# Performance work log

Hardware: AMD Instinct MI355X
Metric: run time of the kernel (lower is better)

Reference implementation:

```python
import jax, jax.numpy as jnp
import numpy as np

B, C, H, W = 2, 64, 128, 128
O = 64
DG = 8          # deformable groups
K = 3
KK = K * K
PAD = 1
MRM = 10.0      # max_residue_magnitude


def setup_inputs() -> dict:
    key = jax.random.key(0)
    ks = jax.random.split(key, 6)
    x0 = jax.random.normal(ks[0], (B, C, H, W), jnp.float32)
    x1 = jax.random.normal(ks[1], (B, C, H, W), jnp.float32)
    pre_offset = jax.random.normal(ks[2], (B, 2 * DG * KK, H, W), jnp.float32)
    pre_sim = jax.random.uniform(ks[3], (B, DG * KK, H, W), jnp.float32)
    stdv = 1.0 / float(np.sqrt(C * KK))
    weight = jax.random.uniform(ks[4], (O, C, K, K), jnp.float32, -stdv, stdv)
    bias = jnp.zeros((O,), jnp.float32)
    # conv_offset_mask params (zero-init in original; small random here so the path is exercised)
    w_om = jax.random.normal(ks[5], (3 * DG * KK, C, K, K), jnp.float32) * 0.01
    b_om = jnp.zeros((3 * DG * KK,), jnp.float32)
    return dict(x0=x0, x1=x1, pre_offset=pre_offset, pre_sim=pre_sim,
                weight=weight, bias=bias, w_om=w_om, b_om=b_om)


def _gather(xg, idx):
    # xg: [BG, cg, HW], idx: [BG, N] int32 -> [BG, cg, N]
    return jax.vmap(lambda a, i: a[:, i])(xg, idx)


def _modulated_deform_conv(x, offset, mask, weight, bias):
    b = x.shape[0]
    cg = C // DG
    # channel layout: ((g*KK + i)*2 + axis), axis 0 = y, 1 = x
    off = offset.reshape(b, DG, KK, 2, H, W)
    m = mask.reshape(b, DG, KK, H, W)
    ky = (jnp.arange(KK) // K).astype(jnp.float32)
    kx = (jnp.arange(KK) % K).astype(jnp.float32)
    base_h = jnp.arange(H, dtype=jnp.float32) - PAD   # stride 1
    base_w = jnp.arange(W, dtype=jnp.float32) - PAD
    py = off[:, :, :, 0] + base_h[None, None, None, :, None] + ky[None, None, :, None, None]
    px = off[:, :, :, 1] + base_w[None, None, None, None, :] + kx[None, None, :, None, None]
    y0 = jnp.floor(py); x0f = jnp.floor(px)
    ly = py - y0; lx = px - x0f
    hy = 1.0 - ly; hx = 1.0 - lx
    y0i = y0.astype(jnp.int32); x0i = x0f.astype(jnp.int32)
    xg = x.reshape(b * DG, cg, H * W)

    def corner(yi, xi, wgt):
        inb = (yi >= 0) & (yi < H) & (xi >= 0) & (xi < W)
        idx = jnp.clip(yi, 0, H - 1) * W + jnp.clip(xi, 0, W - 1)
        g = _gather(xg, idx.reshape(b * DG, KK * H * W))
        g = g.reshape(b, DG, cg, KK, H, W)
        return g * (wgt * inb.astype(x.dtype))[:, :, None]

    val = (corner(y0i, x0i, hy * hx) + corner(y0i, x0i + 1, hy * lx)
           + corner(y0i + 1, x0i, ly * hx) + corner(y0i + 1, x0i + 1, ly * lx))
    val = val * m[:, :, None]                       # modulation mask
    wr = weight.reshape(O, DG, cg, KK)
    out = jnp.einsum('bgckhw,ogck->bohw', val, wr)
    return out + bias[None, :, None, None]


def reference(x0, x1, pre_offset, pre_sim, weight, bias, w_om, b_om):
    # conv_offset_mask on the extra feature x1
    om = jax.lax.conv_general_dilated(x1, w_om, (1, 1), [(PAD, PAD), (PAD, PAD)],
                                      dimension_numbers=('NCHW', 'OIHW', 'NCHW'))
    om = om + b_om[None, :, None, None]
    o1, o2, msk = jnp.split(om, 3, axis=1)
    offset = MRM * jnp.tanh(jnp.concatenate([o1, o2], axis=1)) + pre_offset
    msk = jax.nn.sigmoid(msk * pre_sim)
    return _modulated_deform_conv(x0, offset, msk, weight, bias)
```

## Files before the change

kernel.cpp:

```cpp
#include <hip/hip_runtime.h>
#include <hip/hip_bf16.h>
#include <math.h>

constexpr int B  = 2;
constexpr int C  = 64;
constexpr int H  = 128;
constexpr int W  = 128;
constexpr int O  = 64;
constexpr int DG = 8;
constexpr int K  = 3;
constexpr int KK = K * K;
constexpr int HW = H * W;
constexpr int CG = C / DG;
constexpr int OM_C  = 3 * DG * KK;
constexpr int OFF_C = 2 * DG * KK;
constexpr int MSK_C = DG * KK;
constexpr float MRM = 10.0f;

typedef unsigned short u16;
typedef unsigned int   u32;
typedef short bfx8 __attribute__((ext_vector_type(8)));
typedef short bfx4 __attribute__((ext_vector_type(4)));
typedef float fx4 __attribute__((ext_vector_type(4)));

constexpr int X0T_N  = B * C * HW;
constexpr int WB2_STEP = 7168;
constexpr int WB2_N  = 18 * WB2_STEP;
constexpr int WD_N   = 8 * 3 * 4 * 2 * 512;
constexpr int PW     = 130;
constexpr int PADP   = PW * PW;
constexpr int X1P_N  = B * PADP * C;
constexpr int VKS    = 104;

__device__ constexpr int TAPD[9] = {
    (-PW - 1) * 64, (-PW) * 64, (-PW + 1) * 64,
    (-1) * 64,      0,          (1) * 64,
    (PW - 1) * 64,  (PW) * 64,  (PW + 1) * 64
};

__device__ __forceinline__ float fast_tanh(float x) {
    float e = __expf(2.0f * x);
    return 1.0f - 2.0f * __builtin_amdgcn_rcpf(e + 1.0f);
}
__device__ __forceinline__ float fast_sigmoid(float x) {
    return __builtin_amdgcn_rcpf(1.0f + __expf(-x));
}
__device__ __forceinline__ float bf2f(u16 v) {
    u32 u = ((u32)v) << 16;
    return __builtin_bit_cast(float, u);
}

__global__ void __launch_bounds__(256)
prep1_kernel(const float* __restrict__ weight,
             const float* __restrict__ w_om,
             const float* __restrict__ x1,
             u16* __restrict__ wD,
             u16* __restrict__ x1p_hi,
             u16* __restrict__ x1p_lo,
             u16* __restrict__ wB2) {
    int idx = blockIdx.x * 256 + threadIdx.x;
    if (idx < WD_N) {
        int j    = idx & 7;
        int lane = (idx >> 3) & 63;
        int sel  = (idx >> 9) & 1;
        int nf   = (idx >> 10) & 3;
        int gks  = idx >> 12;
        int g = gks / 3, ks = gks - g * 3;
        int kg = ks * 32 + ((lane >> 4) << 3) + j;
        int oc = nf * 16 + (lane & 15);
        float v = 0.0f;
        if (kg < 72) {
            int i = kg >> 3, c = kg & 7;
            v = weight[oc * (C * KK) + (g * CG + c) * KK + i];
        }
        __hip_bfloat16 hb = __float2bfloat16(v);
        if (sel == 0) {
            wD[idx] = *(u16*)&hb;
        } else {
            float hf = __bfloat162float(hb);
            __hip_bfloat16 lb = __float2bfloat16(v - hf);
            wD[idx] = *(u16*)&lb;
        }
        return;
    }
    int i1 = idx - WD_N;
    if (i1 < B * HW) {
        int p = i1 & (HW - 1);
        int b = i1 >> 14;
        const float* xp = x1 + (size_t)b * C * HW + p;
        bfx8 vh[8], vl[8];
#pragma unroll
        for (int k = 0; k < 8; ++k) {
#pragma unroll
            for (int j = 0; j < 8; ++j) {
                float x = xp[(size_t)(k * 8 + j) * HW];
                __hip_bfloat16 hb = __float2bfloat16(x);
                float hf = __bfloat162float(hb);
                __hip_bfloat16 lb = __float2bfloat16(x - hf);
                vh[k][j] = *(short*)&hb;
                vl[k][j] = *(short*)&lb;
            }
        }
        int dpx = ((p >> 7) + 1) * PW + (p & (W - 1)) + 1;
        u16* dh = x1p_hi + ((size_t)b * PADP + dpx) * C;
        u16* dl = x1p_lo + ((size_t)b * PADP + dpx) * C;
#pragma unroll
        for (int k = 0; k < 8; ++k) {
            *(bfx8*)(dh + k * 8) = vh[k];
            *(bfx8*)(dl + k * 8) = vl[k];
        }
        return;
    }
    int i2 = i1 - B * HW;
    if (i2 < B * PADP) {
        int b2 = i2 / PADP;
        int px = i2 - b2 * PADP;
        int rr = px / PW, cc = px - rr * PW;
        if (rr == 0 || rr == PW - 1 || cc == 0 || cc == PW - 1) {
            u16* zh = x1p_hi + ((size_t)b2 * PADP + px) * C;
            u16* zl = x1p_lo + ((size_t)b2 * PADP + px) * C;
            const bfx8 z = {0, 0, 0, 0, 0, 0, 0, 0};
#pragma unroll
            for (int k = 0; k < 8; ++k) {
                *(bfx8*)(zh + k * 8) = z;
                *(bfx8*)(zl + k * 8) = z;
            }
        }
        return;
    }
    int i3 = i2 - B * PADP;
    if (i3 < WB2_N) {
        int step2 = i3 / WB2_STEP;
        int r     = i3 - step2 * WB2_STEP;
        int nfh  = r >> 9;
        int lane = (r >> 3) & 63;
        int j    = r & 7;
        int t = step2 >> 1, chunk = step2 & 1;
        int ic = chunk * 32 + ((lane >> 4) << 3) + j;
        int oc = (nfh << 4) + (lane & 15);
        float v = (oc < OM_C) ? w_om[oc * (C * KK) + ic * KK + t] : 0.0f;
        __hip_bfloat16 hb = __float2bfloat16(v);
        wB2[i3] = *(u16*)&hb;
    }
}

__global__ void __launch_bounds__(256)
prep2_kernel(const float* __restrict__ x0, u16* __restrict__ x0Tb) {
    int idx = blockIdx.x * 256 + threadIdx.x;
    int p = idx & (HW - 1);
    int g = (idx >> 14) & (DG - 1);
    int b = idx >> 17;
    const float* src = x0 + ((size_t)(b * C + g * CG) * HW) + p;
    bfx8 v;
#pragma unroll
    for (int c = 0; c < CG; ++c) {
        __hip_bfloat16 hb = __float2bfloat16(src[(size_t)c * HW]);
        v[c] = *(short*)&hb;
    }
    *(bfx8*)(x0Tb + (((size_t)(b * DG + g) * HW + p) << 3)) = v;
}

__global__ void __launch_bounds__(1024, 4)
conv_om_mfma_kernel(const u16* __restrict__ x1p_hi,
                    const u16* __restrict__ x1p_lo,
                    const u16* __restrict__ wB2,
                    const float* __restrict__ b_om,
                    float* __restrict__ rawoff,
                    u16* __restrict__ rawmsk16) {
    __shared__ __align__(16) u16 smem[2][2 * WB2_STEP];

    int bid  = blockIdx.x;
    int work = ((bid & 7) << 5) + (bid >> 3);
    int b    = work >> 7;
    int px0  = (work & 127) << 7;

    int tid  = threadIdx.x;
    int lane = tid & 63;
    int wid  = tid >> 6;
    int kidc = wid & 1;
    int wcol = (wid >> 1) & 1;
    int wrow = wid >> 2;

    fx4 acc[2][7];
#pragma unroll
    for (int mf = 0; mf < 2; ++mf)
#pragma unroll
        for (int nf = 0; nf < 7; ++nf) acc[mf][nf] = fx4{0.f, 0.f, 0.f, 0.f};

    int pA    = px0 + wrow * 32 + (lane & 15);
    int klane = (lane >> 4) << 3;
    int base0 = (((pA >> 7) + 1) * PW + (pA & (W - 1)) + 1) * C + kidc * 32 + klane;
    int base1 = base0 + 16 * C;

    const u16* xh_b = x1p_hi + (size_t)b * PADP * C;
    const u16* xl_b = x1p_lo + (size_t)b * PADP * C;

    bool stager = (wid < 14);
    int  soff0 = (wid * 2 + 0) * 512 + lane * 8;
    int  soff1 = (wid * 2 + 1) * 512 + lane * 8;

    if (stager) {
        __builtin_amdgcn_global_load_lds(
            (const __attribute__((address_space(1))) u16*)(wB2 + soff0),
            (__attribute__((address_space(3))) u16*)(&smem[0][0] + soff0), 16, 0, 0);
        __builtin_amdgcn_global_load_lds(
            (const __attribute__((address_space(1))) u16*)(wB2 + soff1),
            (__attribute__((address_space(3))) u16*)(&smem[0][0] + soff1), 16, 0, 0);
    }
    bfx8 ahc0 = *(const bfx8*)(xh_b + base0 + TAPD[0]);
    bfx8 ahc1 = *(const bfx8*)(xh_b + base1 + TAPD[0]);
    bfx8 alc0 = *(const bfx8*)(xl_b + base0 + TAPD[0]);
    bfx8 alc1 = *(const bfx8*)(xl_b + base1 + TAPD[0]);
    __syncthreads();

#pragma unroll
    for (int t = 0; t < 9; ++t) {
        bfx8 ahn0, ahn1, aln0, aln1;
        if (t < 8) {
            if (stager) {
                const u16* src = wB2 + (size_t)(t + 1) * 2 * WB2_STEP;
                u16* dst = &smem[(t + 1) & 1][0];
                __builtin_amdgcn_global_load_lds(
                    (const __attribute__((address_space(1))) u16*)(src + soff0),
                    (__attribute__((address_space(3))) u16*)(dst + soff0), 16, 0, 0);
                __builtin_amdgcn_global_load_lds(
                    (const __attribute__((address_space(1))) u16*)(src + soff1),
                    (__attribute__((address_space(3))) u16*)(dst + soff1), 16, 0, 0);
            }
            int d = TAPD[t + 1];
            ahn0 = *(const bfx8*)(xh_b + base0 + d);
            ahn1 = *(const bfx8*)(xh_b + base1 + d);
            aln0 = *(const bfx8*)(xl_b + base0 + d);
            aln1 = *(const bfx8*)(xl_b + base1 + d);
        }
        const u16* slab = &smem[t & 1][kidc * WB2_STEP];
#pragma unroll
        for (int nf = 0; nf < 7; ++nf) {
            bfx8 bh = *(const bfx8*)(slab + ((wcol * 7 + nf) << 9) + (lane << 3));
            acc[0][nf] = __builtin_amdgcn_mfma_f32_16x16x32_bf16(ahc0, bh, acc[0][nf], 0, 0, 0);
            acc[0][nf] = __builtin_amdgcn_mfma_f32_16x16x32_bf16(alc0, bh, acc[0][nf], 0, 0, 0);
            acc[1][nf] = __builtin_amdgcn_mfma_f32_16x16x32_bf16(ahc1, bh, acc[1][nf], 0, 0, 0);
            acc[1][nf] = __builtin_amdgcn_mfma_f32_16x16x32_bf16(alc1, bh, acc[1][nf], 0, 0, 0);
        }
        __syncthreads();
        if (t < 8) {
            ahc0 = ahn0; ahc1 = ahn1; alc0 = aln0; alc1 = aln1;
        }
    }

    fx4* red = (fx4*)&smem[0][0];
#pragma unroll
    for (int rc = 0; rc < 2; ++rc) {
        if (kidc == 1 && wcol == rc) {
#pragma unroll
            for (int mf = 0; mf < 2; ++mf)
#pragma unroll
                for (int nf = 0; nf < 7; ++nf)
                    red[(((wrow << 1) + mf) * 7 + nf) * 64 + lane] = acc[mf][nf];
        }
        __syncthreads();
        if (kidc == 0 && wcol == rc) {
#pragma unroll
            for (int nf = 0; nf < 7; ++nf) {
#pragma unroll
                for (int mf = 0; mf < 2; ++mf) {
                    fx4 v = acc[mf][nf] + red[(((wrow << 1) + mf) * 7 + nf) * 64 + lane];
                    int oc  = rc * 112 + nf * 16 + (lane & 15);
                    int pix = px0 + wrow * 32 + mf * 16 + ((lane >> 4) << 2);
                    if (oc < OM_C) {
                        float bb = b_om[oc];
                        if (oc < OFF_C) {
                            float4 r;
                            r.x = v[0] + bb; r.y = v[1] + bb;
                            r.z = v[2] + bb; r.w = v[3] + bb;
                            *(float4*)&rawoff[(size_t)(b * OFF_C + oc) * HW + pix] = r;
                        } else {
                            bfx4 rm;
#pragma unroll
                            for (int q = 0; q < 4; ++q) {
                                __hip_bfloat16 hb = __float2bfloat16(v[q] + bb);
                                rm[q] = *(short*)&hb;
                            }
                            *(bfx4*)&rawmsk16[(size_t)(b * MSK_C + oc - OFF_C) * HW + pix] = rm;
                        }
                    }
                }
            }
        }
        __syncthreads();
    }
}

__global__ void __launch_bounds__(256, 4)
deform_mfma_kernel(const u16* __restrict__ x0Tb,
                   const float* __restrict__ rawoff,
                   const u16* __restrict__ rawmsk16,
                   const float* __restrict__ pre_offset,
                   const float* __restrict__ pre_sim,
                   const u16* __restrict__ wD,
                   const float* __restrict__ bias,
                   float* __restrict__ out) {
    __shared__ __align__(16) u16 val[2][2][32][VKS];

    int bid  = blockIdx.x;
    int work = ((bid & 7) << 7) + (bid >> 3);
    int b    = work >> 9;
    int px0  = (work & 511) << 5;

    int tid  = threadIdx.x;
    int lane = tid & 63;
    int nf   = tid >> 6;

    {
        const bfx8 z = {0, 0, 0, 0, 0, 0, 0, 0};
#pragma unroll
        for (int zz = 0; zz < 2; ++zz) {
            int zc = zz * 256 + tid;
            int sub  = zc & 3;
            int rest = zc >> 2;
            int p    = rest & 31;
            int grel = (rest >> 5) & 1;
            int hl   = rest >> 6;
            *(bfx8*)&val[hl][grel][p][72 + sub * 8] = z;
        }
    }

    fx4 acc[2];
    acc[0] = fx4{0.f, 0.f, 0.f, 0.f};
    acc[1] = fx4{0.f, 0.f, 0.f, 0.f};

    for (int r = 0; r < 4; ++r) {
        __syncthreads();
#pragma unroll
        for (int rep = 0; rep < 3; ++rep) {
            int s = rep * 256 + tid;
            if (s < 576) {
                int p    = s & 31;
                int rest = s >> 5;
                int grel = rest / 9;
                int i    = rest - grel * 9;
                int g    = 2 * r + grel;
                int gi   = g * 9 + i;
                int gp   = px0 + p;
                int h = gp >> 7, w = gp & (W - 1);

                size_t oyi = (size_t)(b * OFF_C + 2 * gi) * HW + gp;
                size_t oxi = (size_t)(b * OFF_C + 2 * gi + 1) * HW + gp;
                size_t mii = (size_t)(b * MSK_C + gi) * HW + gp;
                float offy = MRM * fast_tanh(rawoff[oyi]) + pre_offset[oyi];
                float offx = MRM * fast_tanh(rawoff[oxi]) + pre_offset[oxi];
                float m    = fast_sigmoid(bf2f(rawmsk16[mii]) * pre_sim[mii]);

                float py = offy + (float)(h - 1 + i / 3);
                float px = offx + (float)(w - 1 + i % 3);
                float fy = floorf(py), fx = floorf(px);
                float ly = py - fy, lx = px - fx;
                float hy = 1.0f - ly, hx = 1.0f - lx;
                int y0 = (int)fy, x0i = (int)fx;
                int y1 = y0 + 1, x1i = x0i + 1;
                bool vy0 = (y0 >= 0) && (y0 < H);
                bool vy1 = (y1 >= 0) && (y1 < H);
                bool vx0 = (x0i >= 0) && (x0i < W);
                bool vx1 = (x1i >= 0) && (x1i < W);
                int cy0 = min(max(y0, 0), H - 1), cy1 = min(max(y1, 0), H - 1);
                int cx0 = min(max(x0i, 0), W - 1), cx1 = min(max(x1i, 0), W - 1);
                float w00 = hy * hx * ((vy0 && vx0) ? 1.0f : 0.0f) * m;
                float w01 = hy * lx * ((vy0 && vx1) ? 1.0f : 0.0f) * m;
                float w10 = ly * hx * ((vy1 && vx0) ? 1.0f : 0.0f) * m;
                float w11 = ly * lx * ((vy1 && vx1) ? 1.0f : 0.0f) * m;
                int i00 = cy0 * W + cx0, i01 = cy0 * W + cx1;
                int i10 = cy1 * W + cx0, i11 = cy1 * W + cx1;

                const u16* xg = x0Tb + (((size_t)(b * DG + g) * HW) << 3);
                bfx8 c00 = *(const bfx8*)(xg + ((size_t)i00 << 3));
                bfx8 c01 = *(const bfx8*)(xg + ((size_t)i01 << 3));
                bfx8 c10 = *(const bfx8*)(xg + ((size_t)i10 << 3));
                bfx8 c11 = *(const bfx8*)(xg + ((size_t)i11 << 3));

                float v[CG];
#pragma unroll
                for (int c = 0; c < CG; ++c) {
                    v[c] = w00 * bf2f((u16)c00[c]) + w01 * bf2f((u16)c01[c])
                         + w10 * bf2f((u16)c10[c]) + w11 * bf2f((u16)c11[c]);
                }

                bfx8 vh, vl;
#pragma unroll
                for (int c = 0; c < CG; ++c) {
                    __hip_bfloat16 hb = __float2bfloat16(v[c]);
                    float hf = __bfloat162float(hb);
                    __hip_bfloat16 lb = __float2bfloat16(v[c] - hf);
                    vh[c] = *(short*)&hb;
                    vl[c] = *(short*)&lb;
                }
                *(bfx8*)&val[0][grel][p][i * 8] = vh;
                *(bfx8*)&val[1][grel][p][i * 8] = vl;
            }
        }
        __syncthreads();
#pragma unroll
        for (int ks = 0; ks < 6; ++ks) {
            int grel = ks / 3;
            int ksl  = ks - grel * 3;
            int g    = 2 * r + grel;
            int kk   = ksl * 32 + ((lane >> 4) << 3);

            const u16* bp = wD + (size_t)(((g * 3 + ksl) * 4 + nf) * 2) * 512 + lane * 8;
            bfx8 bh = *(const bfx8*)bp;
            bfx8 bl = *(const bfx8*)(bp + 512);

            int row0 = lane & 15;
            bfx8 a0h = *(const bfx8*)&val[0][grel][row0][kk];
            bfx8 a0l = *(const bfx8*)&val[1][grel][row0][kk];
            bfx8 a1h = *(const bfx8*)&val[0][grel][row0 + 16][kk];
            bfx8 a1l = *(const bfx8*)&val[1][grel][row0 + 16][kk];

            acc[0] = __builtin_amdgcn_mfma_f32_16x16x32_bf16(a0h, bh, acc[0], 0, 0, 0);
            acc[0] = __builtin_amdgcn_mfma_f32_16x16x32_bf16(a0l, bh, acc[0], 0, 0, 0);
            acc[0] = __builtin_amdgcn_mfma_f32_16x16x32_bf16(a0h, bl, acc[0], 0, 0, 0);
            acc[1] = __builtin_amdgcn_mfma_f32_16x16x32_bf16(a1h, bh, acc[1], 0, 0, 0);
            acc[1] = __builtin_amdgcn_mfma_f32_16x16x32_bf16(a1l, bh, acc[1], 0, 0, 0);
            acc[1] = __builtin_amdgcn_mfma_f32_16x16x32_bf16(a1h, bl, acc[1], 0, 0, 0);
        }
    }

    __syncthreads();
    float* trans = (float*)&val[0][0][0][0];
#pragma unroll
    for (int t = 0; t < 2; ++t) {
        int oc = nf * 16 + (lane & 15);
        int p4 = t * 16 + ((lane >> 4) << 2);
        *(fx4*)&trans[oc * 36 + p4] = acc[t];
    }
    __syncthreads();
#pragma unroll
    for (int t = 0; t < 2; ++t) {
        int f  = t * 256 + tid;
        int oc = f >> 3;
        int c4 = f & 7;
        float4 v = *(float4*)&trans[oc * 36 + c4 * 4];
        float bb = bias[oc];
        v.x += bb; v.y += bb; v.z += bb; v.w += bb;
        *(float4*)&out[((size_t)b * O + oc) * HW + px0 + c4 * 4] = v;
    }
}

extern "C" void kernel_launch(void* const* d_in, const int* in_sizes, int n_in,
                              void* d_out, int out_size, void* d_ws, size_t ws_size,
                              hipStream_t stream) {
    (void)in_sizes; (void)n_in; (void)out_size; (void)ws_size;
    const float* x0         = (const float*)d_in[0];
    const float* x1         = (const float*)d_in[1];
    const float* pre_offset = (const float*)d_in[2];
    const float* pre_sim    = (const float*)d_in[3];
    const float* weight     = (const float*)d_in[4];
    const float* bias       = (const float*)d_in[5];
    const float* w_om       = (const float*)d_in[6];
    const float* b_om       = (const float*)d_in[7];
    float* out = (float*)d_out;

    float* rawoff   = (float*)d_ws;
    u16*   rawmsk16 = (u16*)(rawoff + (size_t)B * OFF_C * HW);
    u16*   xbuf     = rawmsk16 + (size_t)B * MSK_C * HW;
    u16*   x1p_hi = xbuf;
    u16*   x1p_lo = x1p_hi + (size_t)X1P_N;
    u16*   x0Tb   = xbuf;
    u16*   wB2    = x1p_lo + (size_t)X1P_N;
    u16*   wD     = wB2 + (size_t)WB2_N;

    {
        int total = WD_N + B * HW + B * PADP + WB2_N;
        prep1_kernel<<<(total + 255) / 256, 256, 0, stream>>>(
            weight, w_om, x1, wD, x1p_hi, x1p_lo, wB2);
    }
    {
        conv_om_mfma_kernel<<<256, 1024, 0, stream>>>(
            x1p_hi, x1p_lo, wB2, b_om, rawoff, rawmsk16);
    }
    {
        prep2_kernel<<<(B * DG * HW) / 256, 256, 0, stream>>>(x0, x0Tb);
    }
    {
        deform_mfma_kernel<<<1024, 256, 0, stream>>>(
            x0Tb, rawoff, rawmsk16, pre_offset, pre_sim, wD, bias, out);
    }
}
```

Measured before the change: 79.02 us.

## Shrink conv_om blocks to 256 threads and read weights directly from global

Restructures the offset/mask convolution from 256 blocks of 1024 threads covering 128 pixels into 1024 blocks of 256 threads covering 32 pixels each. It also drops the double-buffered LDS staging of the weight slabs, so each wave loads its B fragments straight from global memory (L2/L1). LDS is now used only for the split-K reduction. The aim is to remove per-tap barriers and the LDS staging overhead and to improve occupancy and scheduling flexibility. In exchange, weight reuse across waves now depends on the caches, and global weight traffic per block rises.

```diff
diff --git a/kernel.cpp b/kernel.cpp
--- a/kernel.cpp
+++ b/kernel.cpp
@@ -160,26 +160,25 @@
     *(bfx8*)(x0Tb + (((size_t)(b * DG + g) * HW + p) << 3)) = v;
 }
 
-__global__ void __launch_bounds__(1024, 4)
+__global__ void __launch_bounds__(256, 4)
 conv_om_mfma_kernel(const u16* __restrict__ x1p_hi,
                     const u16* __restrict__ x1p_lo,
                     const u16* __restrict__ wB2,
                     const float* __restrict__ b_om,
                     float* __restrict__ rawoff,
                     u16* __restrict__ rawmsk16) {
-    __shared__ __align__(16) u16 smem[2][2 * WB2_STEP];
+    __shared__ __align__(16) fx4 red[2][14][64];
 
     int bid  = blockIdx.x;
-    int work = ((bid & 7) << 5) + (bid >> 3);
-    int b    = work >> 7;
-    int px0  = (work & 127) << 7;
+    int work = ((bid & 7) << 7) + (bid >> 3);
+    int b    = work >> 9;
+    int px0  = (work & 511) << 5;
 
     int tid  = threadIdx.x;
     int lane = tid & 63;
     int wid  = tid >> 6;
     int kidc = wid & 1;
-    int wcol = (wid >> 1) & 1;
-    int wrow = wid >> 2;
+    int wcol = wid >> 1;
 
     fx4 acc[2][7];
 #pragma unroll
@@ -187,107 +186,68 @@
 #pragma unroll
         for (int nf = 0; nf < 7; ++nf) acc[mf][nf] = fx4{0.f, 0.f, 0.f, 0.f};
 
-    int pA    = px0 + wrow * 32 + (lane & 15);
+    int pA    = px0 + (lane & 15);
     int klane = (lane >> 4) << 3;
     int base0 = (((pA >> 7) + 1) * PW + (pA & (W - 1)) + 1) * C + kidc * 32 + klane;
     int base1 = base0 + 16 * C;
 
     const u16* xh_b = x1p_hi + (size_t)b * PADP * C;
     const u16* xl_b = x1p_lo + (size_t)b * PADP * C;
-
-    bool stager = (wid < 14);
-    int  soff0 = (wid * 2 + 0) * 512 + lane * 8;
-    int  soff1 = (wid * 2 + 1) * 512 + lane * 8;
-
-    if (stager) {
-        __builtin_amdgcn_global_load_lds(
-            (const __attribute__((address_space(1))) u16*)(wB2 + soff0),
-            (__attribute__((address_space(3))) u16*)(&smem[0][0] + soff0), 16, 0, 0);
-        __builtin_amdgcn_global_load_lds(
-            (const __attribute__((address_space(1))) u16*)(wB2 + soff1),
-            (__attribute__((address_space(3))) u16*)(&smem[0][0] + soff1), 16, 0, 0);
-    }
-    bfx8 ahc0 = *(const bfx8*)(xh_b + base0 + TAPD[0]);
-    bfx8 ahc1 = *(const bfx8*)(xh_b + base1 + TAPD[0]);
-    bfx8 alc0 = *(const bfx8*)(xl_b + base0 + TAPD[0]);
-    bfx8 alc1 = *(const bfx8*)(xl_b + base1 + TAPD[0]);
+    const u16* wbase = wB2 + kidc * WB2_STEP + ((wcol * 7) << 9) + (lane << 3);
+
+#pragma unroll
+    for (int t = 0; t < 9; ++t) {
+        int d = TAPD[t];
+        bfx8 ah0 = *(const bfx8*)(xh_b + base0 + d);
+        bfx8 ah1 = *(const bfx8*)(xh_b + base1 + d);
+        bfx8 al0 = *(const bfx8*)(xl_b + base0 + d);
+        bfx8 al1 = *(const bfx8*)(xl_b + base1 + d);
+        const u16* slab = wbase + (size_t)t * 2 * WB2_STEP;
+#pragma unroll
+        for (int nf = 0; nf < 7; ++nf) {
+            bfx8 bh = *(const bfx8*)(slab + (nf << 9));
+            acc[0][nf] = __builtin_amdgcn_mfma_f32_16x16x32_bf16(ah0, bh, acc[0][nf], 0, 0, 0);
+            acc[0][nf] = __builtin_amdgcn_mfma_f32_16x16x32_bf16(al0, bh, acc[0][nf], 0, 0, 0);
+            acc[1][nf] = __builtin_amdgcn_mfma_f32_16x16x32_bf16(ah1, bh, acc[1][nf], 0, 0, 0);
+            acc[1][nf] = __builtin_amdgcn_mfma_f32_16x16x32_bf16(al1, bh, acc[1][nf], 0, 0, 0);
+        }
+    }
+
+    if (kidc) {
+#pragma unroll
+        for (int mf = 0; mf < 2; ++mf)
+#pragma unroll
+            for (int nf = 0; nf < 7; ++nf)
+                red[wcol][mf * 7 + nf][lane] = acc[mf][nf];
+    }
     __syncthreads();
-
-#pragma unroll
-    for (int t = 0; t < 9; ++t) {
-        bfx8 ahn0, ahn1, aln0, aln1;
-        if (t < 8) {
-            if (stager) {
-                const u16* src = wB2 + (size_t)(t + 1) * 2 * WB2_STEP;
-                u16* dst = &smem[(t + 1) & 1][0];
-                __builtin_amdgcn_global_load_lds(
-                    (const __attribute__((address_space(1))) u16*)(src + soff0),
-                    (__attribute__((address_space(3))) u16*)(dst + soff0), 16, 0, 0);
-                __builtin_amdgcn_global_load_lds(
-                    (const __attribute__((address_space(1))) u16*)(src + soff1),
-                    (__attribute__((address_space(3))) u16*)(dst + soff1), 16, 0, 0);
-            }
-            int d = TAPD[t + 1];
-            ahn0 = *(const bfx8*)(xh_b + base0 + d);
-            ahn1 = *(const bfx8*)(xh_b + base1 + d);
-            aln0 = *(const bfx8*)(xl_b + base0 + d);
-            aln1 = *(const bfx8*)(xl_b + base1 + d);
-        }
-        const u16* slab = &smem[t & 1][kidc * WB2_STEP];
+    if (!kidc) {
 #pragma unroll
         for (int nf = 0; nf < 7; ++nf) {
-            bfx8 bh = *(const bfx8*)(slab + ((wcol * 7 + nf) << 9) + (lane << 3));
-            acc[0][nf] = __builtin_amdgcn_mfma_f32_16x16x32_bf16(ahc0, bh, acc[0][nf], 0, 0, 0);
-            acc[0][nf] = __builtin_amdgcn_mfma_f32_16x16x32_bf16(alc0, bh, acc[0][nf], 0, 0, 0);
-            acc[1][nf] = __builtin_amdgcn_mfma_f32_16x16x32_bf16(ahc1, bh, acc[1][nf], 0, 0, 0);
-            acc[1][nf] = __builtin_amdgcn_mfma_f32_16x16x32_bf16(alc1, bh, acc[1][nf], 0, 0, 0);
-        }
-        __syncthreads();
-        if (t < 8) {
-            ahc0 = ahn0; ahc1 = ahn1; alc0 = aln0; alc1 = aln1;
-        }
-    }
-
-    fx4* red = (fx4*)&smem[0][0];
-#pragma unroll
-    for (int rc = 0; rc < 2; ++rc) {
-        if (kidc == 1 && wcol == rc) {
-#pragma unroll
-            for (int mf = 0; mf < 2; ++mf)
-#pragma unroll
-                for (int nf = 0; nf < 7; ++nf)
-                    red[(((wrow << 1) + mf) * 7 + nf) * 64 + lane] = acc[mf][nf];
-        }
-        __syncthreads();
-        if (kidc == 0 && wcol == rc) {
-#pragma unroll
-            for (int nf = 0; nf < 7; ++nf) {
-#pragma unroll
-                for (int mf = 0; mf < 2; ++mf) {
-                    fx4 v = acc[mf][nf] + red[(((wrow << 1) + mf) * 7 + nf) * 64 + lane];
-                    int oc  = rc * 112 + nf * 16 + (lane & 15);
-                    int pix = px0 + wrow * 32 + mf * 16 + ((lane >> 4) << 2);
-                    if (oc < OM_C) {
-                        float bb = b_om[oc];
-                        if (oc < OFF_C) {
-                            float4 r;
-                            r.x = v[0] + bb; r.y = v[1] + bb;
-                            r.z = v[2] + bb; r.w = v[3] + bb;
-                            *(float4*)&rawoff[(size_t)(b * OFF_C + oc) * HW + pix] = r;
-                        } else {
-                            bfx4 rm;
-#pragma unroll
-                            for (int q = 0; q < 4; ++q) {
-                                __hip_bfloat16 hb = __float2bfloat16(v[q] + bb);
-                                rm[q] = *(short*)&hb;
-                            }
-                            *(bfx4*)&rawmsk16[(size_t)(b * MSK_C + oc - OFF_C) * HW + pix] = rm;
+#pragma unroll
+            for (int mf = 0; mf < 2; ++mf) {
+                fx4 v = acc[mf][nf] + red[wcol][mf * 7 + nf][lane];
+                int oc  = wcol * 112 + nf * 16 + (lane & 15);
+                int pix = px0 + mf * 16 + ((lane >> 4) << 2);
+                if (oc < OM_C) {
+                    float bb = b_om[oc];
+                    if (oc < OFF_C) {
+                        float4 r;
+                        r.x = v[0] + bb; r.y = v[1] + bb;
+                        r.z = v[2] + bb; r.w = v[3] + bb;
+                        *(float4*)&rawoff[(size_t)(b * OFF_C + oc) * HW + pix] = r;
+                    } else {
+                        bfx4 rm;
+#pragma unroll
+                        for (int q = 0; q < 4; ++q) {
+                            __hip_bfloat16 hb = __float2bfloat16(v[q] + bb);
+                            rm[q] = *(short*)&hb;
                         }
+                        *(bfx4*)&rawmsk16[(size_t)(b * MSK_C + oc - OFF_C) * HW + pix] = rm;
                     }
                 }
             }
         }
-        __syncthreads();
     }
 }
 
@@ -474,7 +434,7 @@
             weight, w_om, x1, wD, x1p_hi, x1p_lo, wB2);
     }
     {
-        conv_om_mfma_kernel<<<256, 1024, 0, stream>>>(
+        conv_om_mfma_kernel<<<1024, 256, 0, stream>>>(
             x1p_hi, x1p_lo, wB2, b_om, rawoff, rawmsk16);
     }
     {
```

After: 72.46 us. -8.3%, faster.
